# Optimization experiments

Measured on AMD Instinct MI355X. Metric: run time of the kernel, lower is better.

Reference implementation:

```python
import jax, jax.numpy as jnp
import numpy as np

N, E, G = 20000, 160000, 64
IN_FULL, X_START, X_END = 16, 4, 10
H, OUT, RH, NE, K = 512, 512, 128, 4, 2
NL = 3               # GraphConv layers per expert
SPS, STEMP = 0.3, 1.0  # size_prior_strength, size_temperature


def setup_inputs() -> dict:
    key = jax.random.key(0)
    ks = jax.random.split(key, 10)
    def w(k, shape, fan):
        return jax.random.normal(k, shape, jnp.float32) / np.float32(np.sqrt(fan))
    return dict(
        x=jax.random.normal(ks[0], (N, IN_FULL), jnp.float32),
        edge_index=jax.random.randint(ks[1], (2, E), 0, N),
        batch=jnp.sort(jax.random.randint(ks[2], (N,), 0, G)),
        num_graphs=G,
        enc_W1=w(ks[3], (X_END - X_START, H), X_END - X_START), enc_b1=jnp.zeros((H,), jnp.float32),
        enc_W2=w(ks[4], (H, H), H), enc_b2=jnp.zeros((H,), jnp.float32),
        r_W1=w(ks[5], (H + 2, RH), H + 2), r_b1=jnp.zeros((RH,), jnp.float32),
        ln_g=jnp.ones((RH,), jnp.float32), ln_b=jnp.zeros((RH,), jnp.float32),
        r_W2=w(ks[6], (RH, NE), RH), r_b2=jnp.zeros((NE,), jnp.float32),
        size_centers=jnp.linspace(0.0, 1.0, NE).astype(jnp.float32),
        W_rel=w(ks[7], (NE, NL, H, H), H),       # GraphConv lin_rel weights (stacked)
        b_rel=jnp.zeros((NE, NL, H), jnp.float32),
        W_root=w(ks[8], (NE, NL, H, H), H),      # GraphConv lin_root weights (no bias)
    )


def reference(x, edge_index, batch, num_graphs, enc_W1, enc_b1, enc_W2, enc_b2,
              r_W1, r_b1, ln_g, ln_b, r_W2, r_b2, size_centers, W_rel, b_rel, W_root):
    src, dst = edge_index[0], edge_index[1]
    # encoder: Linear -> ReLU -> Linear on sliced node features
    h = jax.nn.relu(x[:, X_START:X_END] @ enc_W1 + enc_b1) @ enc_W2 + enc_b2
    # per-graph size features (log_nodes_edges mode)
    nodes = jnp.maximum(jax.ops.segment_sum(jnp.ones((N,), x.dtype), batch, num_segments=num_graphs), 1.0)
    edges = jax.ops.segment_sum(jnp.ones((E,), x.dtype), batch[src], num_segments=num_graphs)
    log_n, log_e = jnp.log(nodes), jnp.log1p(edges)
    f = jnp.stack([log_n, log_e], axis=-1)
    f = (f - f.mean(0, keepdims=True)) / (f.std(0, keepdims=True) + 1e-6)
    size_norm = (log_n - log_n.min()) / (log_n.max() - log_n.min() + 1e-6)
    # router: Linear -> LayerNorm -> ReLU -> Linear, plus size prior
    r = jnp.concatenate([h, f[batch]], axis=-1) @ r_W1 + r_b1
    r = (r - r.mean(-1, keepdims=True)) / jnp.sqrt(r.var(-1, keepdims=True) + 1e-5) * ln_g + ln_b
    logits = jax.nn.relu(r) @ r_W2 + r_b2
    prior = -(size_norm[batch][:, None] - size_centers[None, :]) ** 2 / STEMP
    logits = (1.0 - SPS) * logits + SPS * prior
    probs = jax.nn.softmax(logits, axis=-1)
    # top-k sparse gating, renormalized
    v, ix = jax.lax.top_k(probs, K)
    v = v / (v.sum(-1, keepdims=True) + 1e-8)
    weights = jnp.zeros_like(probs).at[jnp.arange(N)[:, None], ix].set(v)  # [N, NE]
    # GraphConv: out_i = (sum_{j->i} z_j) @ W_rel + b_rel + z_i @ W_root
    def gconv(z, Wr, br, Wo):
        agg = jax.ops.segment_sum(z[src], dst, num_segments=N)
        return agg @ Wr + br + z @ Wo
    out = jnp.zeros((N, OUT), x.dtype)
    for e in range(NE):  # small fixed expert count
        z = jax.nn.relu(gconv(h, W_rel[e, 0], b_rel[e, 0], W_root[e, 0]))
        z = jax.nn.relu(gconv(z, W_rel[e, 1], b_rel[e, 1], W_root[e, 1]))
        z = gconv(z, W_rel[e, 2], b_rel[e, 2], W_root[e, 2])
        out = out + weights[:, e:e + 1] * z
    return out
```

## Files before the change

### kernel.cpp

```cpp
#include <hip/hip_runtime.h>
#include <math.h>

#define N_NODES 20000
#define N_EDGES 160000
#define G_GRAPHS 64
#define H_DIM 512
#define RH_DIM 128
#define NE_EXP 4
#define P_ROWS 20096
#define EH_BLOCKS 64

typedef __attribute__((ext_vector_type(8))) short bf16x8;
typedef __attribute__((ext_vector_type(4))) float f32x4;

__device__ __forceinline__ ushort f2bf(float f) {
    uint u = __float_as_uint(f);
    return (ushort)((u + 0x7FFFu + ((u >> 16) & 1u)) >> 16);
}
__device__ __forceinline__ float bf2f(ushort h) {
    return __uint_as_float(((uint)h) << 16);
}

__device__ __forceinline__ void async_copy16(const void* g, void* l) {
    __builtin_amdgcn_global_load_lds(
        (__attribute__((address_space(1))) void*)g,
        (__attribute__((address_space(3))) void*)l, 16, 0, 0);
}

template<int NPASS, bool RELU, int EPI, int NBN>
__global__ __launch_bounds__(256)
void gemm_mfma(const ushort* __restrict__ A0, const ushort* __restrict__ W0,
               const ushort* __restrict__ A1p, const ushort* __restrict__ W1p,
               const ushort* __restrict__ A2p, const ushort* __restrict__ W2p,
               const float* __restrict__ bias, const float* __restrict__ wcol,
               void* __restrict__ out0, void* __restrict__ out1, int Ncols)
{
    __shared__ char smem[32768];
    const int tid = threadIdx.x;
    const int w = tid >> 6, lane = tid & 63;

    const int nwg = gridDim.x;
    const int orig = blockIdx.x;
    const int q = nwg >> 3, r = nwg & 7;
    const int xcd = orig & 7, sid = orig >> 3;
    const int wgid = (xcd < r ? xcd * (q + 1) : r * (q + 1) + (xcd - r) * q) + sid;
    const int m0 = (wgid / NBN) * 128;
    const int n0 = (wgid % NBN) * 128;

    f32x4 acc[4][4];
#pragma unroll
    for (int i = 0; i < 4; ++i)
#pragma unroll
        for (int j = 0; j < 4; ++j) acc[i][j] = (f32x4){0.f, 0.f, 0.f, 0.f};

    const int srow = lane >> 2, schk = lane & 3;
    const int wr = w >> 1, wc = w & 1;
    const int row16 = lane & 15;
    const uint koffB = (uint)(lane >> 4) * 16u;
    const uint aoff0 = (uint)(wr * 64 + row16) * 64u + koffB;
    const uint boff0 = 8192u + (uint)(wc * 64 + row16) * 64u + koffB;

    const int NT = NPASS * 16;
    auto Asel = [&](int t) -> const ushort* { return (t < 16) ? A0 : ((t < 32) ? A1p : A2p); };
    auto Wsel = [&](int t) -> const ushort* { return (t < 16) ? W0 : ((t < 32) ? W1p : W2p); };

    auto stage = [&](int buf, int t) {
        const ushort* __restrict__ A  = Asel(t);
        const ushort* __restrict__ Wt = Wsel(t);
        const int kt = (t & 15) * 32;
        char* base = smem + buf * 16384;
#pragma unroll
        for (int c = 0; c < 2; ++c) {
            const int rb = c * 64 + w * 16;
            async_copy16(A  + (size_t)(m0 + rb + srow) * 512 + kt + schk * 8, base + rb * 64);
            async_copy16(Wt + (size_t)(n0 + rb + srow) * 512 + kt + schk * 8, base + 8192 + rb * 64);
        }
    };
    auto compute = [&](int buf) {
        const char* base = smem + buf * 16384;
        bf16x8 af[4], bfr[4];
#pragma unroll
        for (int i = 0; i < 4; ++i) af[i] = *(const bf16x8*)(base + aoff0 + i * 1024);
#pragma unroll
        for (int j = 0; j < 4; ++j) bfr[j] = *(const bf16x8*)(base + boff0 + j * 1024);
#pragma unroll
        for (int i = 0; i < 4; ++i)
#pragma unroll
            for (int j = 0; j < 4; ++j)
                acc[i][j] = __builtin_amdgcn_mfma_f32_16x16x32_bf16(af[i], bfr[j], acc[i][j], 0, 0, 0);
    };

    stage(0, 0);
    for (int t = 0; t < NT - 1; ++t) {
        stage((t + 1) & 1, t + 1);
        asm volatile("s_waitcnt vmcnt(4)" ::: "memory");
        __builtin_amdgcn_s_barrier();
        compute(t & 1);
        __builtin_amdgcn_s_barrier();
    }
    asm volatile("s_waitcnt vmcnt(0)" ::: "memory");
    __builtin_amdgcn_s_barrier();
    compute((NT - 1) & 1);

#pragma unroll
    for (int i = 0; i < 4; ++i) {
        const int r0 = m0 + wr * 64 + i * 16 + (lane >> 4) * 4;
#pragma unroll
        for (int j = 0; j < 4; ++j) {
            const int c = n0 + wc * 64 + j * 16 + row16;
            const float bj = (EPI == 5) ? 0.f : bias[c];
#pragma unroll
            for (int q2 = 0; q2 < 4; ++q2) {
                const int r = r0 + q2;
                float v = acc[i][j][q2] + bj;
                if (EPI == 0) {
                    if (RELU) v = fmaxf(v, 0.f);
                    ((ushort*)out0)[(size_t)r * Ncols + c] = f2bf(v);
                } else if (EPI == 4) {
                    const ushort hi = f2bf(v);
                    const ushort lo = f2bf(v - bf2f(hi));
                    ((ushort*)out0)[(size_t)r * Ncols + c] = hi;
                    ((ushort*)out1)[(size_t)r * Ncols + c] = lo;
                } else if (EPI == 5) {
                    ((float*)out0)[(size_t)r * Ncols + c] = v;
                } else {
                    if (r < N_NODES) {
                        const float wrow = wcol[(size_t)r * 4];
                        if (EPI == 3) ((float*)out0)[(size_t)r * Ncols + c] = wrow * v;
                        else          ((float*)out0)[(size_t)r * Ncols + c] += wrow * v;
                    }
                }
            }
        }
    }
}

__global__ void encoder1_kernel(const float* __restrict__ x, const float* __restrict__ W1,
                                const float* __restrict__ b1,
                                ushort* __restrict__ t1hi, ushort* __restrict__ t1lo)
{
    const int idx = blockIdx.x * blockDim.x + threadIdx.x;
    if (idx >= P_ROWS * H_DIM) return;
    const int i = idx / H_DIM, j = idx - i * H_DIM;
    float v = 0.f;
    if (i < N_NODES) {
        const float* xr = &x[i * 16 + 4];
        v = b1[j];
#pragma unroll
        for (int k = 0; k < 6; ++k) v = fmaf(xr[k], W1[k * H_DIM + j], v);
        v = fmaxf(v, 0.f);
    }
    const ushort hi = f2bf(v);
    t1hi[idx] = hi;
    t1lo[idx] = f2bf(v - bf2f(hi));
}

__global__ void zero_ints_kernel(int* __restrict__ p, int n)
{
    const int idx = blockIdx.x * blockDim.x + threadIdx.x;
    if (idx < n) p[idx] = 0;
}

__global__ void graph_bounds_kernel(const int* __restrict__ batch, int* __restrict__ gstart)
{
    const int g = threadIdx.x;
    if (g > G_GRAPHS) return;
    int lo = 0, hi = N_NODES;
    while (lo < hi) {
        const int mid = (lo + hi) >> 1;
        if (batch[mid] < g) lo = mid + 1; else hi = mid;
    }
    gstart[g] = lo;
}

__global__ __launch_bounds__(256)
void edge_hist_kernel(const int* __restrict__ src, const int* __restrict__ dst,
                      const int* __restrict__ batch,
                      int* __restrict__ part, int* __restrict__ deg)
{
    __shared__ int hist[G_GRAPHS];
    const int tid = threadIdx.x;
    if (tid < G_GRAPHS) hist[tid] = 0;
    __syncthreads();
    for (int e = blockIdx.x * 256 + tid; e < N_EDGES; e += EH_BLOCKS * 256) {
        atomicAdd(&deg[dst[e]], 1);
        atomicAdd(&hist[batch[src[e]]], 1);
    }
    __syncthreads();
    if (tid < G_GRAPHS) part[blockIdx.x * G_GRAPHS + tid] = hist[tid];
}

__global__ void stats_finalize_kernel(const int* __restrict__ gstart, const int* __restrict__ part,
                                      float* __restrict__ f_norm, float* __restrict__ size_norm)
{
    const int g = threadIdx.x;
    const float nn = fmaxf((float)(gstart[g + 1] - gstart[g]), 1.0f);
    int ec = 0;
#pragma unroll 8
    for (int b = 0; b < EH_BLOCKS; ++b) ec += part[b * G_GRAPHS + g];
    const float ee = (float)ec;
    const float ln = logf(nn);
    const float le = log1pf(ee);
    float s0 = ln, s1 = le;
#pragma unroll
    for (int o = 32; o > 0; o >>= 1) { s0 += __shfl_xor(s0, o); s1 += __shfl_xor(s1, o); }
    const float m0 = s0 / 64.f, m1 = s1 / 64.f;
    const float d0 = ln - m0, d1 = le - m1;
    float v0 = d0 * d0, v1 = d1 * d1;
#pragma unroll
    for (int o = 32; o > 0; o >>= 1) { v0 += __shfl_xor(v0, o); v1 += __shfl_xor(v1, o); }
    const float sd0 = sqrtf(v0 / 64.f), sd1 = sqrtf(v1 / 64.f);
    float mn = ln, mx = ln;
#pragma unroll
    for (int o = 32; o > 0; o >>= 1) {
        mn = fminf(mn, __shfl_xor(mn, o));
        mx = fmaxf(mx, __shfl_xor(mx, o));
    }
    f_norm[g * 2 + 0] = d0 / (sd0 + 1e-6f);
    f_norm[g * 2 + 1] = d1 / (sd1 + 1e-6f);
    size_norm[g] = (ln - mn) / (mx - mn + 1e-6f);
}

__global__ void scan_kernel(const int* __restrict__ in, int* __restrict__ row_ptr,
                            int* __restrict__ cursor, int n)
{
    __shared__ int wsum[16];
    __shared__ int carry_s;
    const int tid = threadIdx.x;
    const int lane = tid & 63, wv = tid >> 6;
    if (tid == 0) carry_s = 0;
    __syncthreads();
    for (int base = 0; base < n; base += 1024) {
        const int idx = base + tid;
        const int v = (idx < n) ? in[idx] : 0;
        int x = v;
#pragma unroll
        for (int o = 1; o < 64; o <<= 1) { const int t = __shfl_up(x, o); if (lane >= o) x += t; }
        if (lane == 63) wsum[wv] = x;
        __syncthreads();
        const int carry = carry_s;
        if (wv == 0) {
            int y = (lane < 16) ? wsum[lane] : 0;
#pragma unroll
            for (int o = 1; o < 16; o <<= 1) { const int t = __shfl_up(y, o); if (lane >= o) y += t; }
            if (lane < 16) wsum[lane] = y;
        }
        __syncthreads();
        const int woff = (wv > 0) ? wsum[wv - 1] : 0;
        const int excl = x - v + woff + carry;
        if (idx < n) { row_ptr[idx] = excl; cursor[idx] = excl; }
        __syncthreads();
        if (tid == 0) carry_s = carry + wsum[15];
        __syncthreads();
    }
    if (tid == 0) row_ptr[n] = carry_s;
}

__global__ void scatter_kernel(const int* __restrict__ src, const int* __restrict__ dst,
                               int* __restrict__ cursor, int* __restrict__ csr_col)
{
    const int e = blockIdx.x * blockDim.x + threadIdx.x;
    if (e >= N_EDGES) return;
    const int d = dst[e];
    const int slot = atomicAdd(&cursor[d], 1);
    csr_col[slot] = src[e];
}

__global__ void sort_adj_kernel(const int* __restrict__ row_ptr, int* __restrict__ csr_col)
{
    const int i = blockIdx.x * blockDim.x + threadIdx.x;
    if (i >= N_NODES) return;
    const int b = row_ptr[i], e = row_ptr[i + 1];
    for (int p = b + 1; p < e; ++p) {
        const int key = csr_col[p];
        int q = p - 1;
        while (q >= b && csr_col[q] > key) { csr_col[q + 1] = csr_col[q]; --q; }
        csr_col[q + 1] = key;
    }
}

__global__ __launch_bounds__(256)
void aggregate_bf16(const uint* __restrict__ z2, const int* __restrict__ row_ptr,
                    const int* __restrict__ csr_col, uint* __restrict__ agg2)
{
    const int i = blockIdx.x;
    const int t = threadIdx.x;
    const int b = row_ptr[i], e = row_ptr[i + 1];
    float ax = 0.f, ay = 0.f;
    int p = b;
    for (; p + 4 <= e; p += 4) {
        const int s0 = csr_col[p + 0], s1 = csr_col[p + 1];
        const int s2 = csr_col[p + 2], s3 = csr_col[p + 3];
        const uint v0 = z2[(size_t)s0 * 256 + t];
        const uint v1 = z2[(size_t)s1 * 256 + t];
        const uint v2 = z2[(size_t)s2 * 256 + t];
        const uint v3 = z2[(size_t)s3 * 256 + t];
        ax += bf2f((ushort)(v0 & 0xffffu)) + bf2f((ushort)(v1 & 0xffffu))
            + bf2f((ushort)(v2 & 0xffffu)) + bf2f((ushort)(v3 & 0xffffu));
        ay += bf2f((ushort)(v0 >> 16)) + bf2f((ushort)(v1 >> 16))
            + bf2f((ushort)(v2 >> 16)) + bf2f((ushort)(v3 >> 16));
    }
    for (; p < e; ++p) {
        const uint v = z2[(size_t)csr_col[p] * 256 + t];
        ax += bf2f((ushort)(v & 0xffffu));
        ay += bf2f((ushort)(v >> 16));
    }
    agg2[(size_t)i * 256 + t] = (uint)f2bf(ax) | ((uint)f2bf(ay) << 16);
}

__global__ __launch_bounds__(256)
void transpose_f32_to_bf16(const float* __restrict__ W, ushort* __restrict__ Wt)
{
    __shared__ float tile[32][33];
    const float* Wm = W + (size_t)blockIdx.z * 512 * 512;
    ushort* Wtm = Wt + (size_t)blockIdx.z * 512 * 512;
    const int c0 = blockIdx.x * 32, r0 = blockIdx.y * 32;
    const int tc = threadIdx.x & 31, tr = threadIdx.x >> 5;
#pragma unroll
    for (int it = 0; it < 4; ++it)
        tile[tr + it * 8][tc] = Wm[(size_t)(r0 + tr + it * 8) * 512 + c0 + tc];
    __syncthreads();
#pragma unroll
    for (int it = 0; it < 4; ++it) {
        const int cr = tr + it * 8;
        Wtm[(size_t)(c0 + cr) * 512 + r0 + tc] = f2bf(tile[tc][cr]);
    }
}

__global__ __launch_bounds__(256)
void transpose_split_kernel(const float* __restrict__ W, ushort* __restrict__ Whi,
                            ushort* __restrict__ Wlo, int Nin)
{
    __shared__ float tile[32][33];
    const int c0 = blockIdx.x * 32;
    const int r0 = blockIdx.y * 32;
    const int tc = threadIdx.x & 31, tr = threadIdx.x >> 5;
#pragma unroll
    for (int it = 0; it < 4; ++it)
        tile[tr + it * 8][tc] = W[(size_t)(r0 + tr + it * 8) * Nin + c0 + tc];
    __syncthreads();
#pragma unroll
    for (int it = 0; it < 4; ++it) {
        const int cr = tr + it * 8;
        const float v = tile[tc][cr];
        const ushort hi = f2bf(v);
        Whi[(size_t)(c0 + cr) * 512 + r0 + tc] = hi;
        Wlo[(size_t)(c0 + cr) * 512 + r0 + tc] = f2bf(v - bf2f(hi));
    }
}

__global__ __launch_bounds__(128)
void router_kernel(const float* __restrict__ rtmp, const int* __restrict__ batch,
                   const float* __restrict__ rW1, const float* __restrict__ rb1,
                   const float* __restrict__ lng, const float* __restrict__ lnb,
                   const float* __restrict__ rW2, const float* __restrict__ rb2,
                   const float* __restrict__ centers,
                   const float* __restrict__ f_norm, const float* __restrict__ size_norm,
                   float* __restrict__ weights)
{
    const int i = blockIdx.x;
    const int j = threadIdx.x;
    const int g = batch[i];
    const float f0 = f_norm[g * 2], f1 = f_norm[g * 2 + 1];
    float r = rtmp[(size_t)i * RH_DIM + j]
            + f0 * rW1[512 * RH_DIM + j] + f1 * rW1[513 * RH_DIM + j] + rb1[j];

    __shared__ float part[2];
    __shared__ float rbuf[RH_DIM];
    __shared__ float lbuf[4];
    const int lane = j & 63, wv = j >> 6;

    float s = r;
#pragma unroll
    for (int o = 32; o > 0; o >>= 1) s += __shfl_xor(s, o);
    if (lane == 0) part[wv] = s;
    __syncthreads();
    const float mean = (part[0] + part[1]) / 128.f;
    __syncthreads();
    const float d = r - mean;
    float v = d * d;
#pragma unroll
    for (int o = 32; o > 0; o >>= 1) v += __shfl_xor(v, o);
    if (lane == 0) part[wv] = v;
    __syncthreads();
    const float var = (part[0] + part[1]) / 128.f;
    const float rn = d / sqrtf(var + 1e-5f) * lng[j] + lnb[j];
    rbuf[j] = fmaxf(rn, 0.f);
    __syncthreads();

    if (j < 4) {
        float acc = rb2[j];
        for (int t = 0; t < RH_DIM; ++t) acc = fmaf(rbuf[t], rW2[t * 4 + j], acc);
        const float sn = size_norm[g];
        const float dd = sn - centers[j];
        lbuf[j] = 0.7f * acc + 0.3f * (-(dd * dd));
    }
    __syncthreads();
    if (j == 0) {
        float p[4];
        const float mx = fmaxf(fmaxf(lbuf[0], lbuf[1]), fmaxf(lbuf[2], lbuf[3]));
#pragma unroll
        for (int c = 0; c < 4; ++c) p[c] = expf(lbuf[c] - mx);
        const float ssum = p[0] + p[1] + p[2] + p[3];
#pragma unroll
        for (int c = 0; c < 4; ++c) p[c] /= ssum;
        int i1 = 0;
#pragma unroll
        for (int c = 1; c < 4; ++c) if (p[c] > p[i1]) i1 = c;
        int i2 = -1;
#pragma unroll
        for (int c = 0; c < 4; ++c) {
            if (c == i1) continue;
            if (i2 < 0 || p[c] > p[i2]) i2 = c;
        }
        const float vs = p[i1] + p[i2] + 1e-8f;
        float wout[4] = {0.f, 0.f, 0.f, 0.f};
        wout[i1] = p[i1] / vs;
        wout[i2] = p[i2] / vs;
#pragma unroll
        for (int c = 0; c < 4; ++c) weights[(size_t)i * 4 + c] = wout[c];
    }
}

extern "C" void kernel_launch(void* const* d_in, const int* in_sizes, int n_in,
                              void* d_out, int out_size, void* d_ws, size_t ws_size,
                              hipStream_t stream)
{
    const float* x       = (const float*)d_in[0];
    const int*   ei      = (const int*)d_in[1];
    const int*   batch   = (const int*)d_in[2];
    const float* enc_W1  = (const float*)d_in[4];
    const float* enc_b1  = (const float*)d_in[5];
    const float* enc_W2  = (const float*)d_in[6];
    const float* enc_b2  = (const float*)d_in[7];
    const float* r_W1    = (const float*)d_in[8];
    const float* r_b1    = (const float*)d_in[9];
    const float* ln_g    = (const float*)d_in[10];
    const float* ln_b    = (const float*)d_in[11];
    const float* r_W2    = (const float*)d_in[12];
    const float* r_b2    = (const float*)d_in[13];
    const float* centers = (const float*)d_in[14];
    const float* W_rel   = (const float*)d_in[15];
    const float* b_rel   = (const float*)d_in[16];
    const float* W_root  = (const float*)d_in[17];
    const int* src = ei;
    const int* dst = ei + N_EDGES;
    float* out = (float*)d_out;

    char* wsp = (char*)d_ws;
    size_t off = 0;
    auto alloc = [&](size_t bytes) -> char* {
        char* p = wsp + off;
        off = (off + bytes + 255) & ~(size_t)255;
        return p;
    };
    const size_t PF = (size_t)P_ROWS * H_DIM;
    char* region1 = alloc(PF * 4);
    ushort* t1hi = (ushort*)region1;
    ushort* t1lo = (ushort*)(region1 + PF * 2);
    ushort* zA16 = (ushort*)region1;
    ushort* zB16 = (ushort*)(region1 + PF * 2);
    float*  rtmp = (float*)region1;
    char* region2 = alloc(PF * 4);
    ushort* h_hi  = (ushort*)region2;
    ushort* h_lo  = (ushort*)(region2 + PF * 2);
    ushort* agg16 = (ushort*)(region2 + PF * 2);
    ushort* aggH16 = (ushort*)alloc(PF * 2);
    ushort* Wt_rel16  = (ushort*)alloc((size_t)12 * 512 * 512 * 2);
    ushort* Wt_root16 = (ushort*)alloc((size_t)12 * 512 * 512 * 2);
    ushort* W2t_hi = (ushort*)alloc((size_t)512 * 512 * 2);
    ushort* W2t_lo = (ushort*)alloc((size_t)512 * 512 * 2);
    ushort* rW1t_hi = (ushort*)alloc((size_t)128 * 512 * 2);
    ushort* rW1t_lo = (ushort*)alloc((size_t)128 * 512 * 2);
    float*  weights   = (float*)alloc((size_t)P_ROWS * 4 * 4);
    int* deg     = (int*)alloc((size_t)N_NODES * 4);
    int* gstart  = (int*)alloc((size_t)(G_GRAPHS + 1) * 4);
    int* part    = (int*)alloc((size_t)EH_BLOCKS * G_GRAPHS * 4);
    int* row_ptr = (int*)alloc((size_t)(N_NODES + 1) * 4);
    int* cursor  = (int*)alloc((size_t)N_NODES * 4);
    int* csr_col = (int*)alloc((size_t)N_EDGES * 4);
    float* f_norm    = (float*)alloc((size_t)G_GRAPHS * 2 * 4);
    float* size_norm = (float*)alloc((size_t)G_GRAPHS * 4);
    (void)ws_size; (void)in_sizes; (void)n_in; (void)out_size;

    const int mfma_nwg   = 4 * (P_ROWS / 128);
    const int mfma_nwg_r = 1 * (P_ROWS / 128);
    const dim3 tr_grid(16, 16, 12);

    zero_ints_kernel<<<(N_NODES + 255) / 256, 256, 0, stream>>>(deg, N_NODES);
    transpose_f32_to_bf16<<<tr_grid, 256, 0, stream>>>(W_rel, Wt_rel16);
    transpose_f32_to_bf16<<<tr_grid, 256, 0, stream>>>(W_root, Wt_root16);
    transpose_split_kernel<<<dim3(16, 16), 256, 0, stream>>>(enc_W2, W2t_hi, W2t_lo, 512);
    transpose_split_kernel<<<dim3(4, 16), 256, 0, stream>>>(r_W1, rW1t_hi, rW1t_lo, 128);
    graph_bounds_kernel<<<1, 128, 0, stream>>>(batch, gstart);
    edge_hist_kernel<<<EH_BLOCKS, 256, 0, stream>>>(src, dst, batch, part, deg);
    stats_finalize_kernel<<<1, 64, 0, stream>>>(gstart, part, f_norm, size_norm);
    encoder1_kernel<<<(P_ROWS * H_DIM + 255) / 256, 256, 0, stream>>>(x, enc_W1, enc_b1, t1hi, t1lo);
    gemm_mfma<3, false, 4, 4><<<mfma_nwg, 256, 0, stream>>>(
        t1hi, W2t_hi, t1hi, W2t_lo, t1lo, W2t_hi, enc_b2, nullptr, h_hi, h_lo, 512);
    gemm_mfma<3, false, 5, 1><<<mfma_nwg_r, 256, 0, stream>>>(
        h_hi, rW1t_hi, h_hi, rW1t_lo, h_lo, rW1t_hi, nullptr, nullptr, rtmp, nullptr, 128);
    router_kernel<<<N_NODES, 128, 0, stream>>>(rtmp, batch, r_W1, r_b1, ln_g, ln_b,
                                               r_W2, r_b2, centers, f_norm, size_norm, weights);
    scan_kernel<<<1, 1024, 0, stream>>>(deg, row_ptr, cursor, N_NODES);
    scatter_kernel<<<(N_EDGES + 255) / 256, 256, 0, stream>>>(src, dst, cursor, csr_col);
    sort_adj_kernel<<<(N_NODES + 255) / 256, 256, 0, stream>>>(row_ptr, csr_col);
    aggregate_bf16<<<N_NODES, 256, 0, stream>>>((const uint*)h_hi, row_ptr, csr_col, (uint*)aggH16);

    for (int e = 0; e < NE_EXP; ++e) {
        const ushort* Wr0 = Wt_rel16  + (size_t)(e * 3 + 0) * 512 * 512;
        const ushort* Wr1 = Wt_rel16  + (size_t)(e * 3 + 1) * 512 * 512;
        const ushort* Wr2 = Wt_rel16  + (size_t)(e * 3 + 2) * 512 * 512;
        const ushort* Wo0 = Wt_root16 + (size_t)(e * 3 + 0) * 512 * 512;
        const ushort* Wo1 = Wt_root16 + (size_t)(e * 3 + 1) * 512 * 512;
        const ushort* Wo2 = Wt_root16 + (size_t)(e * 3 + 2) * 512 * 512;
        const float* br0 = b_rel + (size_t)(e * 3 + 0) * H_DIM;
        const float* br1 = b_rel + (size_t)(e * 3 + 1) * H_DIM;
        const float* br2 = b_rel + (size_t)(e * 3 + 2) * H_DIM;

        gemm_mfma<2, true, 0, 4><<<mfma_nwg, 256, 0, stream>>>(
            aggH16, Wr0, h_hi, Wo0, nullptr, nullptr, br0, nullptr, zA16, nullptr, 512);

        aggregate_bf16<<<N_NODES, 256, 0, stream>>>((const uint*)zA16, row_ptr, csr_col, (uint*)agg16);
        gemm_mfma<2, true, 0, 4><<<mfma_nwg, 256, 0, stream>>>(
            agg16, Wr1, zA16, Wo1, nullptr, nullptr, br1, nullptr, zB16, nullptr, 512);

        aggregate_bf16<<<N_NODES, 256, 0, stream>>>((const uint*)zB16, row_ptr, csr_col, (uint*)agg16);
        if (e == 0) {
            gemm_mfma<2, false, 3, 4><<<mfma_nwg, 256, 0, stream>>>(
                agg16, Wr2, zB16, Wo2, nullptr, nullptr, br2, weights + e, out, nullptr, 512);
        } else {
            gemm_mfma<2, false, 2, 4><<<mfma_nwg, 256, 0, stream>>>(
                agg16, Wr2, zB16, Wo2, nullptr, nullptr, br2, weights + e, out, nullptr, 512);
        }
    }
}
```

Baseline: 932.0 us.

## Batch expert pairs into grouped GEMM and aggregation launches, reduce outputs at end

Processes two experts per launch: a grouped GEMM kernel uses the block index to select expert, and the aggregation kernel gains a grid y dimension for the expert. The final layer writes gate-weighted bf16 per-expert outputs, which a new reduction kernel sums into the fp32 output instead of doing read-modify-write accumulation. This halves the number of launches and doubles the grid size per launch for better GPU fill. The cost is extra workspace buffers and bf16 rounding of the weighted per-expert outputs before summation.

```diff
diff --git a/kernel.cpp b/kernel.cpp
--- a/kernel.cpp
+++ b/kernel.cpp
@@ -9,6 +9,7 @@
 #define NE_EXP 4
 #define P_ROWS 20096
 #define EH_BLOCKS 64
+#define WSZ (512 * 512)
 
 typedef __attribute__((ext_vector_type(8))) short bf16x8;
 typedef __attribute__((ext_vector_type(4))) float f32x4;
@@ -27,25 +28,38 @@
         (__attribute__((address_space(3))) void*)l, 16, 0, 0);
 }
 
-template<int NPASS, bool RELU, int EPI, int NBN>
+__device__ __forceinline__ int xcd_swizzle(int orig, int nwg) {
+    const int q = nwg >> 3, r = nwg & 7;
+    const int xcd = orig & 7, sid = orig >> 3;
+    return (xcd < r ? xcd * (q + 1) : r * (q + 1) + (xcd - r) * q) + sid;
+}
+
+template<bool RELU, int EPI>
 __global__ __launch_bounds__(256)
-void gemm_mfma(const ushort* __restrict__ A0, const ushort* __restrict__ W0,
-               const ushort* __restrict__ A1p, const ushort* __restrict__ W1p,
-               const ushort* __restrict__ A2p, const ushort* __restrict__ W2p,
-               const float* __restrict__ bias, const float* __restrict__ wcol,
-               void* __restrict__ out0, void* __restrict__ out1, int Ncols)
+void gemm_grp(const ushort* __restrict__ A1, size_t a1es,
+              const ushort* __restrict__ W1, size_t w1es,
+              const ushort* __restrict__ A2, size_t a2es,
+              const ushort* __restrict__ W2, size_t w2es,
+              const float* __restrict__ bias, size_t bes,
+              const float* __restrict__ wcol,
+              ushort* __restrict__ out0, size_t oes)
 {
     __shared__ char smem[32768];
     const int tid = threadIdx.x;
     const int w = tid >> 6, lane = tid & 63;
 
-    const int nwg = gridDim.x;
-    const int orig = blockIdx.x;
-    const int q = nwg >> 3, r = nwg & 7;
-    const int xcd = orig & 7, sid = orig >> 3;
-    const int wgid = (xcd < r ? xcd * (q + 1) : r * (q + 1) + (xcd - r) * q) + sid;
-    const int m0 = (wgid / NBN) * 128;
-    const int n0 = (wgid % NBN) * 128;
+    const int wgid = xcd_swizzle(blockIdx.x, gridDim.x);
+    const int m0 = (wgid >> 3) * 128;
+    const int rem = wgid & 7;
+    const int n0 = (rem >> 1) * 128;
+    const int e  = rem & 1;
+
+    const ushort* __restrict__ A1e = A1 + (size_t)e * a1es;
+    const ushort* __restrict__ W1e = W1 + (size_t)e * w1es;
+    const ushort* __restrict__ A2e = A2 + (size_t)e * a2es;
+    const ushort* __restrict__ W2e = W2 + (size_t)e * w2es;
+    const float*  __restrict__ be  = bias + (size_t)e * bes;
+    ushort* __restrict__ oe = out0 + (size_t)e * oes;
 
     f32x4 acc[4][4];
 #pragma unroll
@@ -60,13 +74,9 @@
     const uint aoff0 = (uint)(wr * 64 + row16) * 64u + koffB;
     const uint boff0 = 8192u + (uint)(wc * 64 + row16) * 64u + koffB;
 
-    const int NT = NPASS * 16;
-    auto Asel = [&](int t) -> const ushort* { return (t < 16) ? A0 : ((t < 32) ? A1p : A2p); };
-    auto Wsel = [&](int t) -> const ushort* { return (t < 16) ? W0 : ((t < 32) ? W1p : W2p); };
-
     auto stage = [&](int buf, int t) {
-        const ushort* __restrict__ A  = Asel(t);
-        const ushort* __restrict__ Wt = Wsel(t);
+        const ushort* __restrict__ A  = (t < 16) ? A1e : A2e;
+        const ushort* __restrict__ Wt = (t < 16) ? W1e : W2e;
         const int kt = (t & 15) * 32;
         char* base = smem + buf * 16384;
 #pragma unroll
@@ -91,6 +101,100 @@
     };
 
     stage(0, 0);
+    for (int t = 0; t < 31; ++t) {
+        stage((t + 1) & 1, t + 1);
+        asm volatile("s_waitcnt vmcnt(4)" ::: "memory");
+        __builtin_amdgcn_s_barrier();
+        compute(t & 1);
+        __builtin_amdgcn_s_barrier();
+    }
+    asm volatile("s_waitcnt vmcnt(0)" ::: "memory");
+    __builtin_amdgcn_s_barrier();
+    compute(1);
+
+#pragma unroll
+    for (int i = 0; i < 4; ++i) {
+        const int r0 = m0 + wr * 64 + i * 16 + (lane >> 4) * 4;
+#pragma unroll
+        for (int j = 0; j < 4; ++j) {
+            const int c = n0 + wc * 64 + j * 16 + row16;
+            const float bj = be[c];
+#pragma unroll
+            for (int q2 = 0; q2 < 4; ++q2) {
+                const int r = r0 + q2;
+                float v = acc[i][j][q2] + bj;
+                if (EPI == 0) {
+                    if (RELU) v = fmaxf(v, 0.f);
+                    oe[(size_t)r * 512 + c] = f2bf(v);
+                } else {
+                    const float wrow = (r < N_NODES) ? wcol[(size_t)r * 4 + e] : 0.f;
+                    oe[(size_t)r * 512 + c] = f2bf(v * wrow);
+                }
+            }
+        }
+    }
+}
+
+template<int NPASS, int EPI, int NBN>
+__global__ __launch_bounds__(256)
+void gemm_mfma(const ushort* __restrict__ A0, const ushort* __restrict__ W0,
+               const ushort* __restrict__ A1p, const ushort* __restrict__ W1p,
+               const ushort* __restrict__ A2p, const ushort* __restrict__ W2p,
+               const float* __restrict__ bias,
+               void* __restrict__ out0, void* __restrict__ out1, int Ncols)
+{
+    __shared__ char smem[32768];
+    const int tid = threadIdx.x;
+    const int w = tid >> 6, lane = tid & 63;
+
+    const int wgid = xcd_swizzle(blockIdx.x, gridDim.x);
+    const int m0 = (wgid / NBN) * 128;
+    const int n0 = (wgid % NBN) * 128;
+
+    f32x4 acc[4][4];
+#pragma unroll
+    for (int i = 0; i < 4; ++i)
+#pragma unroll
+        for (int j = 0; j < 4; ++j) acc[i][j] = (f32x4){0.f, 0.f, 0.f, 0.f};
+
+    const int srow = lane >> 2, schk = lane & 3;
+    const int wr = w >> 1, wc = w & 1;
+    const int row16 = lane & 15;
+    const uint koffB = (uint)(lane >> 4) * 16u;
+    const uint aoff0 = (uint)(wr * 64 + row16) * 64u + koffB;
+    const uint boff0 = 8192u + (uint)(wc * 64 + row16) * 64u + koffB;
+
+    const int NT = NPASS * 16;
+    auto Asel = [&](int t) -> const ushort* { return (t < 16) ? A0 : ((t < 32) ? A1p : A2p); };
+    auto Wsel = [&](int t) -> const ushort* { return (t < 16) ? W0 : ((t < 32) ? W1p : W2p); };
+
+    auto stage = [&](int buf, int t) {
+        const ushort* __restrict__ A  = Asel(t);
+        const ushort* __restrict__ Wt = Wsel(t);
+        const int kt = (t & 15) * 32;
+        char* base = smem + buf * 16384;
+#pragma unroll
+        for (int c = 0; c < 2; ++c) {
+            const int rb = c * 64 + w * 16;
+            async_copy16(A  + (size_t)(m0 + rb + srow) * 512 + kt + schk * 8, base + rb * 64);
+            async_copy16(Wt + (size_t)(n0 + rb + srow) * 512 + kt + schk * 8, base + 8192 + rb * 64);
+        }
+    };
+    auto compute = [&](int buf) {
+        const char* base = smem + buf * 16384;
+        bf16x8 af[4], bfr[4];
+#pragma unroll
+        for (int i = 0; i < 4; ++i) af[i] = *(const bf16x8*)(base + aoff0 + i * 1024);
+#pragma unroll
+        for (int j = 0; j < 4; ++j) bfr[j] = *(const bf16x8*)(base + boff0 + j * 1024);
+#pragma unroll
+        for (int i = 0; i < 4; ++i)
+#pragma unroll
+            for (int j = 0; j < 4; ++j)
+                acc[i][j] = __builtin_amdgcn_mfma_f32_16x16x32_bf16(af[i], bfr[j], acc[i][j], 0, 0, 0);
+    };
+
+    stage(0, 0);
     for (int t = 0; t < NT - 1; ++t) {
         stage((t + 1) & 1, t + 1);
         asm volatile("s_waitcnt vmcnt(4)" ::: "memory");
@@ -113,26 +217,32 @@
             for (int q2 = 0; q2 < 4; ++q2) {
                 const int r = r0 + q2;
                 float v = acc[i][j][q2] + bj;
-                if (EPI == 0) {
-                    if (RELU) v = fmaxf(v, 0.f);
-                    ((ushort*)out0)[(size_t)r * Ncols + c] = f2bf(v);
-                } else if (EPI == 4) {
+                if (EPI == 4) {
                     const ushort hi = f2bf(v);
                     const ushort lo = f2bf(v - bf2f(hi));
                     ((ushort*)out0)[(size_t)r * Ncols + c] = hi;
                     ((ushort*)out1)[(size_t)r * Ncols + c] = lo;
-                } else if (EPI == 5) {
+                } else {
                     ((float*)out0)[(size_t)r * Ncols + c] = v;
-                } else {
-                    if (r < N_NODES) {
-                        const float wrow = wcol[(size_t)r * 4];
-                        if (EPI == 3) ((float*)out0)[(size_t)r * Ncols + c] = wrow * v;
-                        else          ((float*)out0)[(size_t)r * Ncols + c] += wrow * v;
-                    }
                 }
             }
         }
     }
+}
+
+__global__ __launch_bounds__(256)
+void reduce_wz_kernel(const uint* __restrict__ wz01, const uint* __restrict__ wz23,
+                      float2* __restrict__ out)
+{
+    const size_t idx = (size_t)blockIdx.x * 256 + threadIdx.x;
+    const size_t es = (size_t)P_ROWS * 256;
+    const uint a = wz01[idx], b = wz01[idx + es];
+    const uint c = wz23[idx], d = wz23[idx + es];
+    float lo = bf2f((ushort)(a & 0xffffu)) + bf2f((ushort)(b & 0xffffu))
+             + bf2f((ushort)(c & 0xffffu)) + bf2f((ushort)(d & 0xffffu));
+    float hi = bf2f((ushort)(a >> 16)) + bf2f((ushort)(b >> 16))
+             + bf2f((ushort)(c >> 16)) + bf2f((ushort)(d >> 16));
+    out[idx] = make_float2(lo, hi);
 }
 
 __global__ void encoder1_kernel(const float* __restrict__ x, const float* __restrict__ W1,
@@ -283,6 +393,9 @@
 void aggregate_bf16(const uint* __restrict__ z2, const int* __restrict__ row_ptr,
                     const int* __restrict__ csr_col, uint* __restrict__ agg2)
 {
+    const size_t es = (size_t)blockIdx.y * P_ROWS * 256;
+    const uint* __restrict__ zz = z2 + es;
+    uint* __restrict__ aa = agg2 + es;
     const int i = blockIdx.x;
     const int t = threadIdx.x;
     const int b = row_ptr[i], e = row_ptr[i + 1];
@@ -291,29 +404,29 @@
     for (; p + 4 <= e; p += 4) {
         const int s0 = csr_col[p + 0], s1 = csr_col[p + 1];
         const int s2 = csr_col[p + 2], s3 = csr_col[p + 3];
-        const uint v0 = z2[(size_t)s0 * 256 + t];
-        const uint v1 = z2[(size_t)s1 * 256 + t];
-        const uint v2 = z2[(size_t)s2 * 256 + t];
-        const uint v3 = z2[(size_t)s3 * 256 + t];
+        const uint v0 = zz[(size_t)s0 * 256 + t];
+        const uint v1 = zz[(size_t)s1 * 256 + t];
+        const uint v2 = zz[(size_t)s2 * 256 + t];
+        const uint v3 = zz[(size_t)s3 * 256 + t];
         ax += bf2f((ushort)(v0 & 0xffffu)) + bf2f((ushort)(v1 & 0xffffu))
             + bf2f((ushort)(v2 & 0xffffu)) + bf2f((ushort)(v3 & 0xffffu));
         ay += bf2f((ushort)(v0 >> 16)) + bf2f((ushort)(v1 >> 16))
             + bf2f((ushort)(v2 >> 16)) + bf2f((ushort)(v3 >> 16));
     }
     for (; p < e; ++p) {
-        const uint v = z2[(size_t)csr_col[p] * 256 + t];
+        const uint v = zz[(size_t)csr_col[p] * 256 + t];
         ax += bf2f((ushort)(v & 0xffffu));
         ay += bf2f((ushort)(v >> 16));
     }
-    agg2[(size_t)i * 256 + t] = (uint)f2bf(ax) | ((uint)f2bf(ay) << 16);
+    aa[(size_t)i * 256 + t] = (uint)f2bf(ax) | ((uint)f2bf(ay) << 16);
 }
 
 __global__ __launch_bounds__(256)
 void transpose_f32_to_bf16(const float* __restrict__ W, ushort* __restrict__ Wt)
 {
     __shared__ float tile[32][33];
-    const float* Wm = W + (size_t)blockIdx.z * 512 * 512;
-    ushort* Wtm = Wt + (size_t)blockIdx.z * 512 * 512;
+    const float* Wm = W + (size_t)blockIdx.z * WSZ;
+    ushort* Wtm = Wt + (size_t)blockIdx.z * WSZ;
     const int c0 = blockIdx.x * 32, r0 = blockIdx.y * 32;
     const int tc = threadIdx.x & 31, tr = threadIdx.x >> 5;
 #pragma unroll
@@ -455,24 +568,29 @@
         return p;
     };
     const size_t PF = (size_t)P_ROWS * H_DIM;
-    char* region1 = alloc(PF * 4);
-    ushort* t1hi = (ushort*)region1;
-    ushort* t1lo = (ushort*)(region1 + PF * 2);
-    ushort* zA16 = (ushort*)region1;
-    ushort* zB16 = (ushort*)(region1 + PF * 2);
-    float*  rtmp = (float*)region1;
-    char* region2 = alloc(PF * 4);
-    ushort* h_hi  = (ushort*)region2;
-    ushort* h_lo  = (ushort*)(region2 + PF * 2);
-    ushort* agg16 = (ushort*)(region2 + PF * 2);
+    char* B_t1 = alloc(PF * 4);
+    ushort* t1hi = (ushort*)B_t1;
+    ushort* t1lo = (ushort*)(B_t1 + PF * 2);
+    ushort* wz01 = (ushort*)B_t1;
+    char* B_h = alloc(PF * 4);
+    ushort* h_hi = (ushort*)B_h;
+    ushort* h_lo = (ushort*)(B_h + PF * 2);
+    ushort* wz23 = (ushort*)B_h;
+    char* B_zA = alloc(PF * 4);
+    ushort* zA2 = (ushort*)B_zA;
+    float*  rtmp = (float*)B_zA;
+    char* B_zB = alloc(PF * 4);
+    ushort* zB2 = (ushort*)B_zB;
+    char* B_ag = alloc(PF * 4);
+    ushort* agg2 = (ushort*)B_ag;
     ushort* aggH16 = (ushort*)alloc(PF * 2);
-    ushort* Wt_rel16  = (ushort*)alloc((size_t)12 * 512 * 512 * 2);
-    ushort* Wt_root16 = (ushort*)alloc((size_t)12 * 512 * 512 * 2);
-    ushort* W2t_hi = (ushort*)alloc((size_t)512 * 512 * 2);
-    ushort* W2t_lo = (ushort*)alloc((size_t)512 * 512 * 2);
+    ushort* Wt_rel16  = (ushort*)alloc((size_t)12 * WSZ * 2);
+    ushort* Wt_root16 = (ushort*)alloc((size_t)12 * WSZ * 2);
+    ushort* W2t_hi = (ushort*)alloc((size_t)WSZ * 2);
+    ushort* W2t_lo = (ushort*)alloc((size_t)WSZ * 2);
     ushort* rW1t_hi = (ushort*)alloc((size_t)128 * 512 * 2);
     ushort* rW1t_lo = (ushort*)alloc((size_t)128 * 512 * 2);
-    float*  weights   = (float*)alloc((size_t)P_ROWS * 4 * 4);
+    float*  weights = (float*)alloc((size_t)P_ROWS * 4 * 4);
     int* deg     = (int*)alloc((size_t)N_NODES * 4);
     int* gstart  = (int*)alloc((size_t)(G_GRAPHS + 1) * 4);
     int* part    = (int*)alloc((size_t)EH_BLOCKS * G_GRAPHS * 4);
@@ -483,9 +601,11 @@
     float* size_norm = (float*)alloc((size_t)G_GRAPHS * 4);
     (void)ws_size; (void)in_sizes; (void)n_in; (void)out_size;
 
-    const int mfma_nwg   = 4 * (P_ROWS / 128);
-    const int mfma_nwg_r = 1 * (P_ROWS / 128);
+    const int enc_nwg = 4 * (P_ROWS / 128);
+    const int rtr_nwg = 1 * (P_ROWS / 128);
+    const int grp_nwg = 8 * (P_ROWS / 128);
     const dim3 tr_grid(16, 16, 12);
+    const dim3 agg_grid1(N_NODES, 1), agg_grid2(N_NODES, 2);
 
     zero_ints_kernel<<<(N_NODES + 255) / 256, 256, 0, stream>>>(deg, N_NODES);
     transpose_f32_to_bf16<<<tr_grid, 256, 0, stream>>>(W_rel, Wt_rel16);
@@ -496,42 +616,36 @@
     edge_hist_kernel<<<EH_BLOCKS, 256, 0, stream>>>(src, dst, batch, part, deg);
     stats_finalize_kernel<<<1, 64, 0, stream>>>(gstart, part, f_norm, size_norm);
     encoder1_kernel<<<(P_ROWS * H_DIM + 255) / 256, 256, 0, stream>>>(x, enc_W1, enc_b1, t1hi, t1lo);
-    gemm_mfma<3, false, 4, 4><<<mfma_nwg, 256, 0, stream>>>(
-        t1hi, W2t_hi, t1hi, W2t_lo, t1lo, W2t_hi, enc_b2, nullptr, h_hi, h_lo, 512);
-    gemm_mfma<3, false, 5, 1><<<mfma_nwg_r, 256, 0, stream>>>(
-        h_hi, rW1t_hi, h_hi, rW1t_lo, h_lo, rW1t_hi, nullptr, nullptr, rtmp, nullptr, 128);
+    gemm_mfma<3, 4, 4><<<enc_nwg, 256, 0, stream>>>(
+        t1hi, W2t_hi, t1hi, W2t_lo, t1lo, W2t_hi, enc_b2, h_hi, h_lo, 512);
+    gemm_mfma<3, 5, 1><<<rtr_nwg, 256, 0, stream>>>(
+        h_hi, rW1t_hi, h_hi, rW1t_lo, h_lo, rW1t_hi, nullptr, rtmp, nullptr, 128);
     router_kernel<<<N_NODES, 128, 0, stream>>>(rtmp, batch, r_W1, r_b1, ln_g, ln_b,
                                                r_W2, r_b2, centers, f_norm, size_norm, weights);
     scan_kernel<<<1, 1024, 0, stream>>>(deg, row_ptr, cursor, N_NODES);
     scatter_kernel<<<(N_EDGES + 255) / 256, 256, 0, stream>>>(src, dst, cursor, csr_col);
     sort_adj_kernel<<<(N_NODES + 255) / 256, 256, 0, stream>>>(row_ptr, csr_col);
-    aggregate_bf16<<<N_NODES, 256, 0, stream>>>((const uint*)h_hi, row_ptr, csr_col, (uint*)aggH16);
-
-    for (int e = 0; e < NE_EXP; ++e) {
-        const ushort* Wr0 = Wt_rel16  + (size_t)(e * 3 + 0) * 512 * 512;
-        const ushort* Wr1 = Wt_rel16  + (size_t)(e * 3 + 1) * 512 * 512;
-        const ushort* Wr2 = Wt_rel16  + (size_t)(e * 3 + 2) * 512 * 512;
-        const ushort* Wo0 = Wt_root16 + (size_t)(e * 3 + 0) * 512 * 512;
-        const ushort* Wo1 = Wt_root16 + (size_t)(e * 3 + 1) * 512 * 512;
-        const ushort* Wo2 = Wt_root16 + (size_t)(e * 3 + 2) * 512 * 512;
-        const float* br0 = b_rel + (size_t)(e * 3 + 0) * H_DIM;
-        const float* br1 = b_rel + (size_t)(e * 3 + 1) * H_DIM;
-        const float* br2 = b_rel + (size_t)(e * 3 + 2) * H_DIM;
-
-        gemm_mfma<2, true, 0, 4><<<mfma_nwg, 256, 0, stream>>>(
-            aggH16, Wr0, h_hi, Wo0, nullptr, nullptr, br0, nullptr, zA16, nullptr, 512);
-
-        aggregate_bf16<<<N_NODES, 256, 0, stream>>>((const uint*)zA16, row_ptr, csr_col, (uint*)agg16);
-        gemm_mfma<2, true, 0, 4><<<mfma_nwg, 256, 0, stream>>>(
-            agg16, Wr1, zA16, Wo1, nullptr, nullptr, br1, nullptr, zB16, nullptr, 512);
-
-        aggregate_bf16<<<N_NODES, 256, 0, stream>>>((const uint*)zB16, row_ptr, csr_col, (uint*)agg16);
-        if (e == 0) {
-            gemm_mfma<2, false, 3, 4><<<mfma_nwg, 256, 0, stream>>>(
-                agg16, Wr2, zB16, Wo2, nullptr, nullptr, br2, weights + e, out, nullptr, 512);
-        } else {
-            gemm_mfma<2, false, 2, 4><<<mfma_nwg, 256, 0, stream>>>(
-                agg16, Wr2, zB16, Wo2, nullptr, nullptr, br2, weights + e, out, nullptr, 512);
-        }
-    }
-}
+    aggregate_bf16<<<agg_grid1, 256, 0, stream>>>((const uint*)h_hi, row_ptr, csr_col, (uint*)aggH16);
+
+    const size_t WES = (size_t)3 * WSZ;
+    const size_t BES = (size_t)3 * 512;
+    for (int p = 0; p < 2; ++p) {
+        const size_t eb = (size_t)(p * 2);
+        const ushort* WrP = Wt_rel16  + eb * WES;
+        const ushort* WoP = Wt_root16 + eb * WES;
+        const float*  brP = b_rel + eb * BES;
+        ushort* wzP = (p == 0) ? wz01 : wz23;
+
+        gemm_grp<true, 0><<<grp_nwg, 256, 0, stream>>>(
+            aggH16, 0, WrP, WES, h_hi, 0, WoP, WES, brP, BES, nullptr, zA2, PF);
+        aggregate_bf16<<<agg_grid2, 256, 0, stream>>>((const uint*)zA2, row_ptr, csr_col, (uint*)agg2);
+        gemm_grp<true, 0><<<grp_nwg, 256, 0, stream>>>(
+            agg2, PF, WrP + WSZ, WES, zA2, PF, WoP + WSZ, WES, brP + 512, BES, nullptr, zB2, PF);
+        aggregate_bf16<<<agg_grid2, 256, 0, stream>>>((const uint*)zB2, row_ptr, csr_col, (uint*)agg2);
+        gemm_grp<false, 6><<<grp_nwg, 256, 0, stream>>>(
+            agg2, PF, WrP + 2 * WSZ, WES, zB2, PF, WoP + 2 * WSZ, WES, brP + 1024, BES,
+            weights + eb, wzP, PF);
+    }
+    reduce_wz_kernel<<<N_NODES, 256, 0, stream>>>((const uint*)wz01, (const uint*)wz23,
+                                                  (float2*)out);
+}
```

Measured after the change: 863.0 us. 1.08x faster.
